# Optimization experiments

Hardware: AMD Instinct MI355X
Metric: run time of the kernel (lower is better)

Reference implementation:

```python
import jax, jax.numpy as jnp
import numpy as np

# dims
N, E, C, KV, H, OUT, MID, L = 8192, 32768, 32, 8, 8, 16, 64, 2
KVT = 2 * KV          # fused key+value channels per degree
EDGE_DIM = 5          # 4 edge scalar channels + radial norm (get_populated_edge_features)
S = KVT * C           # radial weight block per (pair, frequency)
RAD_OUT = 6 * S       # pairs (0,0),(0,1),(1,0) x1 freq + (1,1) x3 freqs

_EPS3 = np.zeros((3, 3, 3), np.float32)
for (a, b, c) in [(0, 1, 2), (1, 2, 0), (2, 0, 1)]:
    _EPS3[a, b, c] = 1.0
for (a, b, c) in [(0, 2, 1), (2, 1, 0), (1, 0, 2)]:
    _EPS3[a, b, c] = -1.0


def _ln(x, g, b):
    mu = x.mean(-1, keepdims=True)
    v = ((x - mu) ** 2).mean(-1, keepdims=True)
    return (x - mu) / jnp.sqrt(v + 1e-5) * g + b


def _radial(es, W1, b1, g, beta, W2):
    # radial profile MLP with layer norm (use_layer_norm=True)
    return jax.nn.relu(_ln(es @ W1 + b1, g, beta)) @ W2


def _segment_softmax(logit, dst, n):
    mx = jax.ops.segment_max(logit, dst, n)
    z = jnp.exp(logit - mx[dst])
    den = jax.ops.segment_sum(z, dst, n)
    return z / (den[dst] + 1e-9)


def reference(node_feats_0, node_feats_1, edge_feats_0, rel_pos, scale, src, dst,
              rad_W1, rad_b1, rad_g, rad_beta, rad_W2, Wq0, Wq1, Wp0, Wp1,
              ng0, nb0, ng1, nb1, fin_W1, fin_b1, fin_g, fin_beta, fin_W2):
    eps3 = jnp.asarray(_EPS3)
    e, n = rel_pos.shape[0], node_feats_0.shape[0]
    # --- get_basis: spherical-harmonic / Clebsch-Gordan basis up to max_degree=1 ---
    rn = jnp.linalg.norm(rel_pos, axis=-1, keepdims=True)           # [E,1]
    rhat = rel_pos / (rn + 1e-12)                                    # [E,3]
    I3 = jnp.eye(3, dtype=rel_pos.dtype)
    Q0 = jnp.broadcast_to(I3 / jnp.sqrt(3.0), (e, 3, 3))             # J=0 for 1->1
    Q1 = jnp.einsum('abc,ec->eab', eps3, rhat) / jnp.sqrt(2.0)       # J=1 for 1->1
    Q2 = jnp.sqrt(1.5) * (rhat[:, :, None] * rhat[:, None, :] - I3 / 3.0)  # J=2
    Q11 = jnp.stack([Q0, Q1, Q2], axis=1)                            # [E,3,3,3]
    es = jnp.concatenate([rn, edge_feats_0[:, :, 0]], axis=-1)       # [E,5]
    f0, f1 = node_feats_0, node_feats_1
    for i in range(L):
        # --- ConvSE3 producing fused key||value per degree ---
        R = _radial(es, rad_W1[i], rad_b1[i], rad_g[i], rad_beta[i], rad_W2[i])
        R00 = R[:, :S].reshape(e, KVT, C)
        R01 = R[:, S:2 * S].reshape(e, KVT, C)
        R10 = R[:, 2 * S:3 * S].reshape(e, KVT, C)
        R11 = R[:, 3 * S:].reshape(e, 3, KVT, C)
        f0s, f1s = f0[src], f1[src]
        m0 = (jnp.einsum('eoc,ec->eo', R00, f0s[:, :, 0])
              + jnp.einsum('eoc,eb,ecb->eo', R10, rhat, f1s))          # [E,KVT]
        m1 = (jnp.einsum('eoc,ea,ec->eoa', R01, rhat, f0s[:, :, 0])
              + jnp.einsum('ejoc,ejab,ecb->eoa', R11, Q11, f1s))       # [E,KVT,3]
        m0 = m0 * scale[:, None]
        m1 = m1 * scale[:, None, None]
        # --- attention: keys from edges, queries from dst nodes ---
        k = jnp.concatenate([m0[:, :KV], m1[:, :KV].reshape(e, KV * 3)], -1).reshape(e, H, -1)
        q0 = jnp.einsum('ncm,ck->nkm', f0, Wq0[i])                     # [N,KV,1]
        q1 = jnp.einsum('ncm,ck->nkm', f1, Wq1[i])                     # [N,KV,3]
        q = jnp.concatenate([q0[:, :, 0], q1.reshape(n, KV * 3)], -1).reshape(n, H, -1)
        logit = (k * q[dst]).sum(-1) / np.sqrt(k.shape[-1])            # [E,H]
        a = _segment_softmax(logit, dst, n)
        v0 = m0[:, KV:].reshape(e, H, KV // H)
        v1 = m1[:, KV:].reshape(e, H, KV // H, 3)
        o0 = jax.ops.segment_sum(a[:, :, None] * v0, dst, n).reshape(n, KV, 1)
        o1 = jax.ops.segment_sum(a[:, :, None, None] * v1, dst, n).reshape(n, KV, 3)
        # --- project (attn out concat skip) ---
        f0 = jnp.einsum('ncm,co->nom', jnp.concatenate([o0, f0], 1), Wp0[i])
        f1 = jnp.einsum('ncm,co->nom', jnp.concatenate([o1, f1], 1), Wp1[i])
        # --- NormSE3: equivariant norm-gated nonlinearity ---
        n0 = jnp.sqrt((f0 ** 2).sum(-1) + 1e-12)
        f0 = f0 * (jax.nn.relu(_ln(n0, ng0[i], nb0[i])) / n0)[:, :, None]
        n1 = jnp.sqrt((f1 ** 2).sum(-1) + 1e-12)
        f1 = f1 * (jax.nn.relu(_ln(n1, ng1[i], nb1[i])) / n1)[:, :, None]
    # --- final ConvSE3 (pool=False, self_interaction=False) -> degree 0 ---
    Rf = _radial(es, fin_W1, fin_b1, fin_g, fin_beta, fin_W2)
    Rf00 = Rf[:, :OUT * C].reshape(e, OUT, C)
    Rf10 = Rf[:, OUT * C:].reshape(e, OUT, C)
    mf = (jnp.einsum('eoc,ec->eo', Rf00, f0[src][:, :, 0])
          + jnp.einsum('eoc,eb,ecb->eo', Rf10, rhat, f1[src])) * scale[:, None]
    return jax.ops.segment_sum(mf, dst, n)[:, :, None]                 # feats['0']: [N,OUT,1]


def setup_inputs():
    ks = jax.random.split(jax.random.key(0), 16)
    s = 0.1
    d = {}
    d['node_feats_0'] = jax.random.normal(ks[0], (N, C, 1), jnp.float32)
    d['node_feats_1'] = jax.random.normal(ks[1], (N, C, 3), jnp.float32)
    d['edge_feats_0'] = jax.random.normal(ks[2], (E, 4, 1), jnp.float32)
    d['rel_pos'] = jax.random.normal(ks[3], (E, 3), jnp.float32)
    d['scale'] = jax.random.uniform(ks[4], (E,), jnp.float32)
    d['src'] = jax.random.randint(ks[5], (E,), 0, N)
    d['dst'] = jax.random.randint(ks[6], (E,), 0, N)
    d['rad_W1'] = jax.random.normal(ks[7], (L, EDGE_DIM, MID), jnp.float32) * s
    d['rad_b1'] = jnp.zeros((L, MID), jnp.float32)
    d['rad_g'] = jnp.ones((L, MID), jnp.float32)
    d['rad_beta'] = jnp.zeros((L, MID), jnp.float32)
    d['rad_W2'] = jax.random.normal(ks[8], (L, MID, RAD_OUT), jnp.float32) * (s / 8)
    d['Wq0'] = jax.random.normal(ks[9], (L, C, KV), jnp.float32) * s
    d['Wq1'] = jax.random.normal(ks[10], (L, C, KV), jnp.float32) * s
    d['Wp0'] = jax.random.normal(ks[11], (L, KV + C, C), jnp.float32) * s
    d['Wp1'] = jax.random.normal(ks[12], (L, KV + C, C), jnp.float32) * s
    d['ng0'] = jnp.ones((L, C), jnp.float32)
    d['nb0'] = jnp.zeros((L, C), jnp.float32)
    d['ng1'] = jnp.ones((L, C), jnp.float32)
    d['nb1'] = jnp.zeros((L, C), jnp.float32)
    d['fin_W1'] = jax.random.normal(ks[13], (EDGE_DIM, MID), jnp.float32) * s
    d['fin_b1'] = jnp.zeros((MID,), jnp.float32)
    d['fin_g'] = jnp.ones((MID,), jnp.float32)
    d['fin_beta'] = jnp.zeros((MID,), jnp.float32)
    d['fin_W2'] = jax.random.normal(ks[14], (MID, 2 * OUT * C), jnp.float32) * (s / 8)
    return d
```

## Files before the change

kernel.cpp:

```cpp
#include <hip/hip_runtime.h>
#include <math.h>

#define NN 8192
#define NE 32768
#define CC 32
#define EB 64

typedef __attribute__((ext_vector_type(8))) short s16x8;
typedef __attribute__((ext_vector_type(4))) float f32x4;

__device__ __forceinline__ unsigned short f2bf(float f) {
  unsigned u = __float_as_uint(f);
  u += 0x7FFFu + ((u >> 16) & 1u);
  return (unsigned short)(u >> 16);
}

__device__ __forceinline__ void mfma_pair(const s16x8* __restrict__ w2v, int g, int lane,
                                          s16x8 bh0, s16x8 bh1, f32x4& D0, f32x4& D1) {
  const s16x8* ap = w2v + ((size_t)g*4*64 + lane);
  s16x8 a00 = ap[0], a01 = ap[64], a10 = ap[128], a11 = ap[192];
  f32x4 z = {0.f,0.f,0.f,0.f};
  D0 = __builtin_amdgcn_mfma_f32_16x16x32_bf16(a00, bh0, z, 0,0,0);
  D0 = __builtin_amdgcn_mfma_f32_16x16x32_bf16(a01, bh1, D0, 0,0,0);
  D1 = __builtin_amdgcn_mfma_f32_16x16x32_bf16(a10, bh0, z, 0,0,0);
  D1 = __builtin_amdgcn_mfma_f32_16x16x32_bf16(a11, bh1, D1, 0,0,0);
}

__global__ void k_prep(const float* __restrict__ rel, const float* __restrict__ ef,
                       float* __restrict__ es, float* __restrict__ rhat) {
  int e = blockIdx.x * blockDim.x + threadIdx.x;
  if (e >= NE) return;
  float x = rel[e*3+0], y = rel[e*3+1], z = rel[e*3+2];
  float rn = sqrtf(x*x + y*y + z*z);
  float inv = 1.0f / (rn + 1e-12f);
  rhat[e*3+0] = x*inv; rhat[e*3+1] = y*inv; rhat[e*3+2] = z*inv;
  es[e*5+0] = rn;
  es[e*5+1] = ef[e*4+0];
  es[e*5+2] = ef[e*4+1];
  es[e*5+3] = ef[e*4+2];
  es[e*5+4] = ef[e*4+3];
}

__global__ void k_count(const int* __restrict__ dst, int* __restrict__ cnt) {
  int e = blockIdx.x * blockDim.x + threadIdx.x;
  if (e < NE) atomicAdd(&cnt[dst[e]], 1);
}

__global__ __launch_bounds__(1024) void k_scan(const int* __restrict__ cnt,
                                               int* __restrict__ offs, int* __restrict__ cursor) {
  __shared__ int part[1024];
  int t = threadIdx.x;
  int base = t * 8;
  int loc[8];
  int s = 0;
  #pragma unroll
  for (int j = 0; j < 8; ++j) { loc[j] = s; s += cnt[base + j]; }
  part[t] = s;
  __syncthreads();
  for (int off = 1; off < 1024; off <<= 1) {
    int v = (t >= off) ? part[t - off] : 0;
    __syncthreads();
    part[t] += v;
    __syncthreads();
  }
  int pre = (t == 0) ? 0 : part[t - 1];
  #pragma unroll
  for (int j = 0; j < 8; ++j) {
    int o = pre + loc[j];
    offs[base + j] = o;
    cursor[base + j] = o;
  }
  if (t == 1023) offs[NN] = part[1023];
}

__global__ void k_fill(const int* __restrict__ dst, int* __restrict__ cursor,
                       int* __restrict__ eidx) {
  int e = blockIdx.x * blockDim.x + threadIdx.x;
  if (e >= NE) return;
  int pos = atomicAdd(&cursor[dst[e]], 1);
  eidx[pos] = e;
}

__global__ void k_radial(const float* __restrict__ es, const float* __restrict__ W1,
                         const float* __restrict__ b1, const float* __restrict__ g,
                         const float* __restrict__ be, unsigned short* __restrict__ h) {
  int t = blockIdx.x * blockDim.x + threadIdx.x;
  int e = t >> 6, m = t & 63;
  if (e >= NE) return;
  const float* ep = es + (size_t)e*5;
  float v = b1[m];
  v = fmaf(ep[0], W1[0*64+m], v);
  v = fmaf(ep[1], W1[1*64+m], v);
  v = fmaf(ep[2], W1[2*64+m], v);
  v = fmaf(ep[3], W1[3*64+m], v);
  v = fmaf(ep[4], W1[4*64+m], v);
  float s = v;
  #pragma unroll
  for (int off = 32; off; off >>= 1) s += __shfl_xor(s, off);
  float mu = s * (1.0f/64.0f);
  float d = v - mu;
  float s2 = d*d;
  #pragma unroll
  for (int off = 32; off; off >>= 1) s2 += __shfl_xor(s2, off);
  float hv = d * rsqrtf(s2*(1.0f/64.0f) + 1e-5f) * g[m] + be[m];
  h[(size_t)e*64+m] = f2bf(fmaxf(hv, 0.0f));
}

__global__ void k_w2cvt(const float* __restrict__ W2, unsigned short* __restrict__ dstp, int N) {
  int idx = blockIdx.x * blockDim.x + threadIdx.x;
  int total = (N >> 5) * 4 * 64;
  if (idx >= total) return;
  int l = idx & 63;
  int fr = idx >> 6;
  int kh = fr & 1;
  int mt = (fr >> 1) & 1;
  int g  = fr >> 2;
  int kb  = kh*32 + (l >> 4)*8;
  int col = g*32 + mt*16 + (l & 15);
  s16x8 v;
  #pragma unroll
  for (int j = 0; j < 8; ++j) v[j] = (short)f2bf(W2[(size_t)(kb + j)*N + col]);
  *reinterpret_cast<s16x8*>(dstp + (size_t)idx*8) = v;
}

__global__ __launch_bounds__(512) void k_conv_mfma(
    const unsigned short* __restrict__ hbf, const unsigned short* __restrict__ w2s,
    const float* __restrict__ f0, const float* __restrict__ f1,
    const float* __restrict__ rhat, const float* __restrict__ scale,
    const int* __restrict__ src, float* __restrict__ m_out)
{
  __shared__ float rhs[EB][4];
  __shared__ float scs[EB];
  __shared__ float macc[EB][81];
  int tid = threadIdx.x;
  int e0 = blockIdx.x * EB;

  for (int idx = tid; idx < EB; idx += 512) {
    rhs[idx][0] = rhat[(e0+idx)*3+0];
    rhs[idx][1] = rhat[(e0+idx)*3+1];
    rhs[idx][2] = rhat[(e0+idx)*3+2];
    scs[idx]    = scale[e0+idx];
  }

  int lane = tid & 63, wv = tid >> 6;
  int cl = lane & 15;
  int rb = ((lane >> 4) & 3) * 4;
  int ko = (lane >> 4) * 8;
  int et = wv & 3, gp = wv >> 2;
  int e  = et*16 + cl;

  const unsigned short* hb = hbf + (size_t)e0*64;
  s16x8 bh0 = *reinterpret_cast<const s16x8*>(hb + (size_t)e*64 + ko);
  s16x8 bh1 = *reinterpret_cast<const s16x8*>(hb + (size_t)e*64 + 32 + ko);
  const s16x8* w2v = reinterpret_cast<const s16x8*>(w2s);

  int sn = src[e0+e];
  float rx = rhat[(e0+e)*3+0], ry = rhat[(e0+e)*3+1], rz = rhat[(e0+e)*3+2];
  float F0[8], T1[8], F1r[24];
  #pragma unroll
  for (int r = 0; r < 4; ++r) {
    int cA = rb + r, cB = 16 + rb + r;
    F0[r]   = f0[(size_t)sn*32 + cA];
    F0[4+r] = f0[(size_t)sn*32 + cB];
    #pragma unroll
    for (int a = 0; a < 3; ++a) {
      F1r[r*3+a]    = f1[(size_t)sn*96 + cA*3 + a];
      F1r[12+r*3+a] = f1[(size_t)sn*96 + cB*3 + a];
    }
  }
  #pragma unroll
  for (int r = 0; r < 4; ++r) {
    T1[r]   = rx*F1r[r*3+0]    + ry*F1r[r*3+1]    + rz*F1r[r*3+2];
    T1[4+r] = rx*F1r[12+r*3+0] + ry*F1r[12+r*3+1] + rz*F1r[12+r*3+2];
  }

  const float inv_s3 = 0.57735026919f;
  const float inv_s2 = 0.70710678118f;
  const float c15    = 1.22474487139f;

  #pragma unroll 1
  for (int i = 0; i < 8; ++i) {
    int g = 2*i + gp;
    float m0v, qv, m1x, m1y, m1z;
    {
      f32x4 D0, D1;
      mfma_pair(w2v, g, lane, bh0, bh1, D0, D1);
      float p = 0.f;
      #pragma unroll
      for (int r = 0; r < 4; ++r) { p = fmaf(D0[r], F0[r], p); p = fmaf(D1[r], F0[4+r], p); }
      m0v = p;
    }
    {
      f32x4 D0, D1;
      mfma_pair(w2v, 16 + g, lane, bh0, bh1, D0, D1);
      float p = 0.f;
      #pragma unroll
      for (int r = 0; r < 4; ++r) { p = fmaf(D0[r], F0[r], p); p = fmaf(D1[r], F0[4+r], p); }
      qv = p;
    }
    {
      f32x4 D0, D1;
      mfma_pair(w2v, 32 + g, lane, bh0, bh1, D0, D1);
      float p = 0.f;
      #pragma unroll
      for (int r = 0; r < 4; ++r) { p = fmaf(D0[r], T1[r], p); p = fmaf(D1[r], T1[4+r], p); }
      m0v += p;
    }
    {
      f32x4 D0, D1;
      mfma_pair(w2v, 48 + g, lane, bh0, bh1, D0, D1);
      float v0=0.f, v1=0.f, v2=0.f;
      #pragma unroll
      for (int r = 0; r < 4; ++r) {
        v0 = fmaf(D0[r], F1r[r*3+0], v0); v0 = fmaf(D1[r], F1r[12+r*3+0], v0);
        v1 = fmaf(D0[r], F1r[r*3+1], v1); v1 = fmaf(D1[r], F1r[12+r*3+1], v1);
        v2 = fmaf(D0[r], F1r[r*3+2], v2); v2 = fmaf(D1[r], F1r[12+r*3+2], v2);
      }
      m1x = v0*inv_s3; m1y = v1*inv_s3; m1z = v2*inv_s3;
    }
    {
      f32x4 D0, D1;
      mfma_pair(w2v, 64 + g, lane, bh0, bh1, D0, D1);
      float v0=0.f, v1=0.f, v2=0.f;
      #pragma unroll
      for (int r = 0; r < 4; ++r) {
        v0 = fmaf(D0[r], F1r[r*3+0], v0); v0 = fmaf(D1[r], F1r[12+r*3+0], v0);
        v1 = fmaf(D0[r], F1r[r*3+1], v1); v1 = fmaf(D1[r], F1r[12+r*3+1], v1);
        v2 = fmaf(D0[r], F1r[r*3+2], v2); v2 = fmaf(D1[r], F1r[12+r*3+2], v2);
      }
      m1x += (rz*v1 - ry*v2)*inv_s2;
      m1y += (rx*v2 - rz*v0)*inv_s2;
      m1z += (ry*v0 - rx*v1)*inv_s2;
    }
    {
      f32x4 D0, D1;
      mfma_pair(w2v, 80 + g, lane, bh0, bh1, D0, D1);
      float v0=0.f, v1=0.f, v2=0.f, w=0.f;
      #pragma unroll
      for (int r = 0; r < 4; ++r) {
        v0 = fmaf(D0[r], F1r[r*3+0], v0); v0 = fmaf(D1[r], F1r[12+r*3+0], v0);
        v1 = fmaf(D0[r], F1r[r*3+1], v1); v1 = fmaf(D1[r], F1r[12+r*3+1], v1);
        v2 = fmaf(D0[r], F1r[r*3+2], v2); v2 = fmaf(D1[r], F1r[12+r*3+2], v2);
        w  = fmaf(D0[r], T1[r], w);       w  = fmaf(D1[r], T1[4+r], w);
      }
      m1x += c15*(rx*w - v0*(1.0f/3.0f));
      m1y += c15*(ry*w - v1*(1.0f/3.0f));
      m1z += c15*(rz*w - v2*(1.0f/3.0f));
    }
    m0v += __shfl_xor(m0v, 16); m0v += __shfl_xor(m0v, 32);
    qv  += __shfl_xor(qv,  16); qv  += __shfl_xor(qv,  32);
    m1x += __shfl_xor(m1x, 16); m1x += __shfl_xor(m1x, 32);
    m1y += __shfl_xor(m1y, 16); m1y += __shfl_xor(m1y, 32);
    m1z += __shfl_xor(m1z, 16); m1z += __shfl_xor(m1z, 32);
    if (lane < 16) {
      macc[e][g]          = m0v;
      macc[e][16 + g]     = qv;
      macc[e][32 + g*3+0] = m1x;
      macc[e][32 + g*3+1] = m1y;
      macc[e][32 + g*3+2] = m1z;
    }
  }
  __syncthreads();
  for (int idx = tid; idx < EB*64; idx += 512) {
    int e2 = idx >> 6, t2 = idx & 63;
    float sc = scs[e2];
    float val;
    if (t2 < 16) {
      val = macc[e2][t2] * sc;
    } else {
      int o = (t2-16)/3, a2 = (t2-16)%3;
      val = (macc[e2][32 + (t2-16)] + macc[e2][16+o]*rhs[e2][a2]) * sc;
    }
    m_out[(size_t)(e0+e2)*64 + t2] = val;
  }
}

__global__ void k_query(const float* __restrict__ f0, const float* __restrict__ f1,
                        const float* __restrict__ Wq0, const float* __restrict__ Wq1,
                        float* __restrict__ q) {
  int n = blockIdx.x * blockDim.x + threadIdx.x;
  if (n >= NN) return;
  float q0[8]  = {0,0,0,0,0,0,0,0};
  float q1x[8] = {0,0,0,0,0,0,0,0};
  float q1y[8] = {0,0,0,0,0,0,0,0};
  float q1z[8] = {0,0,0,0,0,0,0,0};
  for (int c = 0; c < 32; ++c) {
    float fv = f0[(size_t)n*32+c];
    float fx = f1[(size_t)n*96+c*3+0];
    float fy = f1[(size_t)n*96+c*3+1];
    float fz = f1[(size_t)n*96+c*3+2];
    #pragma unroll
    for (int k = 0; k < 8; ++k) {
      float w0 = Wq0[c*8+k], w1 = Wq1[c*8+k];
      q0[k]  = fmaf(fv, w0, q0[k]);
      q1x[k] = fmaf(fx, w1, q1x[k]);
      q1y[k] = fmaf(fy, w1, q1y[k]);
      q1z[k] = fmaf(fz, w1, q1z[k]);
    }
  }
  #pragma unroll
  for (int k = 0; k < 8; ++k) {
    q[(size_t)n*32+k]         = q0[k];
    q[(size_t)n*32+8+k*3+0]   = q1x[k];
    q[(size_t)n*32+8+k*3+1]   = q1y[k];
    q[(size_t)n*32+8+k*3+2]   = q1z[k];
  }
}

__global__ void k_attn(const float* __restrict__ m, const float* __restrict__ q,
                       const int* __restrict__ offs, const int* __restrict__ eidx,
                       float* __restrict__ o0, float* __restrict__ o1) {
  int idx = blockIdx.x * blockDim.x + threadIdx.x;
  int n = idx >> 3, h = idx & 7;
  if (n >= NN) return;
  const float* qd = q + (size_t)n*32 + 4*h;
  float q0 = qd[0], q1 = qd[1], q2 = qd[2], q3 = qd[3];
  int kb = (h < 2) ? 4*h : 8 + 4*h;
  int b0 = offs[n], b1 = offs[n+1];
  float M = -3.4e38f, D = 0.f, A0 = 0.f, Ax = 0.f, Ay = 0.f, Az = 0.f;
  for (int j = b0; j < b1; ++j) {
    int e = eidx[j];
    const float* me = m + (size_t)e*64;
    float4 kv = *reinterpret_cast<const float4*>(me + kb);
    float l = 0.5f * (kv.x*q0 + kv.y*q1 + kv.z*q2 + kv.w*q3);
    float v0 = me[8+h];
    float vx = me[40+3*h], vy = me[41+3*h], vz = me[42+3*h];
    if (l > M) {
      float sc = __expf(M - l);
      D *= sc; A0 *= sc; Ax *= sc; Ay *= sc; Az *= sc;
      M = l;
    }
    float z = __expf(l - M);
    D += z;
    A0 = fmaf(z, v0, A0);
    Ax = fmaf(z, vx, Ax);
    Ay = fmaf(z, vy, Ay);
    Az = fmaf(z, vz, Az);
  }
  float inv = 1.0f / (D + 1e-9f);
  o0[(size_t)n*8+h] = A0*inv;
  o1[(size_t)n*24+3*h+0] = Ax*inv;
  o1[(size_t)n*24+3*h+1] = Ay*inv;
  o1[(size_t)n*24+3*h+2] = Az*inv;
}

__global__ void k_update(const float* __restrict__ o0, const float* __restrict__ o1,
                         const float* __restrict__ f0c, const float* __restrict__ f1c,
                         const float* __restrict__ Wp0, const float* __restrict__ Wp1,
                         const float* __restrict__ ng0v, const float* __restrict__ nb0v,
                         const float* __restrict__ ng1v, const float* __restrict__ nb1v,
                         float* __restrict__ f0o, float* __restrict__ f1o) {
  int t = blockIdx.x * blockDim.x + threadIdx.x;
  int n = t >> 5, o = t & 31;
  if (n >= NN) return;
  float a0 = 0.0f, ax = 0.0f, ay = 0.0f, az = 0.0f;
  for (int c = 0; c < 8; ++c) {
    float w0 = Wp0[c*32+o], w1 = Wp1[c*32+o];
    a0 = fmaf(o0[(size_t)n*8+c], w0, a0);
    ax = fmaf(o1[(size_t)n*24+c*3+0], w1, ax);
    ay = fmaf(o1[(size_t)n*24+c*3+1], w1, ay);
    az = fmaf(o1[(size_t)n*24+c*3+2], w1, az);
  }
  for (int c = 0; c < 32; ++c) {
    float w0 = Wp0[(8+c)*32+o], w1 = Wp1[(8+c)*32+o];
    a0 = fmaf(f0c[(size_t)n*32+c], w0, a0);
    ax = fmaf(f1c[(size_t)n*96+c*3+0], w1, ax);
    ay = fmaf(f1c[(size_t)n*96+c*3+1], w1, ay);
    az = fmaf(f1c[(size_t)n*96+c*3+2], w1, az);
  }
  float nn0 = sqrtf(a0*a0 + 1e-12f);
  float nn1 = sqrtf(ax*ax + ay*ay + az*az + 1e-12f);
  float s0 = nn0, s1 = nn1;
  #pragma unroll
  for (int off = 16; off; off >>= 1) { s0 += __shfl_xor(s0, off, 32); s1 += __shfl_xor(s1, off, 32); }
  float mu0 = s0*(1.0f/32.0f), mu1 = s1*(1.0f/32.0f);
  float d0 = nn0 - mu0, d1 = nn1 - mu1;
  float v0 = d0*d0, v1 = d1*d1;
  #pragma unroll
  for (int off = 16; off; off >>= 1) { v0 += __shfl_xor(v0, off, 32); v1 += __shfl_xor(v1, off, 32); }
  float g0 = fmaxf(d0*rsqrtf(v0*(1.0f/32.0f)+1e-5f)*ng0v[o] + nb0v[o], 0.0f) / nn0;
  float g1 = fmaxf(d1*rsqrtf(v1*(1.0f/32.0f)+1e-5f)*ng1v[o] + nb1v[o], 0.0f) / nn1;
  f0o[(size_t)n*32+o] = a0*g0;
  f1o[(size_t)n*96+o*3+0] = ax*g1;
  f1o[(size_t)n*96+o*3+1] = ay*g1;
  f1o[(size_t)n*96+o*3+2] = az*g1;
}

__global__ __launch_bounds__(512) void k_fconv_mfma(
    const unsigned short* __restrict__ hbf, const unsigned short* __restrict__ w2s,
    const float* __restrict__ f0, const float* __restrict__ f1,
    const float* __restrict__ rhat, const float* __restrict__ scale,
    const int* __restrict__ src, const int* __restrict__ dst, float* __restrict__ out)
{
  __shared__ float macc[EB][17];
  __shared__ float scs[EB];
  int tid = threadIdx.x;
  int e0 = blockIdx.x * EB;

  for (int idx = tid; idx < EB; idx += 512) scs[idx] = scale[e0+idx];

  int lane = tid & 63, wv = tid >> 6;
  int cl = lane & 15;
  int rb = ((lane >> 4) & 3) * 4;
  int ko = (lane >> 4) * 8;
  int et = wv & 3, gp = wv >> 2;
  int e  = et*16 + cl;

  const unsigned short* hb = hbf + (size_t)e0*64;
  s16x8 bh0 = *reinterpret_cast<const s16x8*>(hb + (size_t)e*64 + ko);
  s16x8 bh1 = *reinterpret_cast<const s16x8*>(hb + (size_t)e*64 + 32 + ko);
  const s16x8* w2v = reinterpret_cast<const s16x8*>(w2s);

  int sn = src[e0+e];
  float rx = rhat[(e0+e)*3+0], ry = rhat[(e0+e)*3+1], rz = rhat[(e0+e)*3+2];
  float F0[8], T1[8];
  #pragma unroll
  for (int r = 0; r < 4; ++r) {
    int cA = rb + r, cB = 16 + rb + r;
    F0[r]   = f0[(size_t)sn*32 + cA];
    F0[4+r] = f0[(size_t)sn*32 + cB];
    float ax0 = f1[(size_t)sn*96 + cA*3 + 0];
    float ax1 = f1[(size_t)sn*96 + cA*3 + 1];
    float ax2 = f1[(size_t)sn*96 + cA*3 + 2];
    float bx0 = f1[(size_t)sn*96 + cB*3 + 0];
    float bx1 = f1[(size_t)sn*96 + cB*3 + 1];
    float bx2 = f1[(size_t)sn*96 + cB*3 + 2];
    T1[r]   = rx*ax0 + ry*ax1 + rz*ax2;
    T1[4+r] = rx*bx0 + ry*bx1 + rz*bx2;
  }

  #pragma unroll 1
  for (int i = 0; i < 8; ++i) {
    int g = 2*i + gp;
    float am;
    {
      f32x4 D0, D1;
      mfma_pair(w2v, g, lane, bh0, bh1, D0, D1);
      float p = 0.f;
      #pragma unroll
      for (int r = 0; r < 4; ++r) { p = fmaf(D0[r], F0[r], p); p = fmaf(D1[r], F0[4+r], p); }
      am = p;
    }
    {
      f32x4 D0, D1;
      mfma_pair(w2v, 16 + g, lane, bh0, bh1, D0, D1);
      float p = 0.f;
      #pragma unroll
      for (int r = 0; r < 4; ++r) { p = fmaf(D0[r], T1[r], p); p = fmaf(D1[r], T1[4+r], p); }
      am += p;
    }
    am += __shfl_xor(am, 16); am += __shfl_xor(am, 32);
    if (lane < 16) macc[e][g] = am;
  }
  __syncthreads();
  for (int idx = tid; idx < EB*16; idx += 512) {
    int e2 = idx >> 4, o = idx & 15;
    atomicAdd(&out[(size_t)dst[e0+e2]*16 + o], macc[e2][o]*scs[e2]);
  }
}

extern "C" void kernel_launch(void* const* d_in, const int* in_sizes, int n_in,
                              void* d_out, int out_size, void* d_ws, size_t ws_size,
                              hipStream_t stream) {
  (void)in_sizes; (void)n_in; (void)ws_size;
  const float* nf0  = (const float*)d_in[0];
  const float* nf1  = (const float*)d_in[1];
  const float* ef0  = (const float*)d_in[2];
  const float* rel  = (const float*)d_in[3];
  const float* scale= (const float*)d_in[4];
  const int*   src  = (const int*)d_in[5];
  const int*   dst  = (const int*)d_in[6];
  const float* rW1  = (const float*)d_in[7];
  const float* rb1  = (const float*)d_in[8];
  const float* rg   = (const float*)d_in[9];
  const float* rbe  = (const float*)d_in[10];
  const float* rW2  = (const float*)d_in[11];
  const float* Wq0  = (const float*)d_in[12];
  const float* Wq1  = (const float*)d_in[13];
  const float* Wp0  = (const float*)d_in[14];
  const float* Wp1  = (const float*)d_in[15];
  const float* ng0  = (const float*)d_in[16];
  const float* nb0  = (const float*)d_in[17];
  const float* ng1  = (const float*)d_in[18];
  const float* nb1  = (const float*)d_in[19];
  const float* fW1  = (const float*)d_in[20];
  const float* fb1  = (const float*)d_in[21];
  const float* fg   = (const float*)d_in[22];
  const float* fbe  = (const float*)d_in[23];
  const float* fW2  = (const float*)d_in[24];

  float* ws = (float*)d_ws;
  size_t off = 0;
  float* es    = ws + off; off += (size_t)NE*5;
  float* rhat  = ws + off; off += (size_t)NE*3;
  float* m     = ws + off; off += (size_t)NE*64;
  float* q     = ws + off; off += (size_t)NN*32;
  float* o0    = ws + off; off += (size_t)NN*8;
  float* o1    = ws + off; off += (size_t)NN*24;
  float* f0a   = ws + off; off += (size_t)NN*32;
  float* f1a   = ws + off; off += (size_t)NN*96;
  float* f0b   = ws + off; off += (size_t)NN*32;
  float* f1b   = ws + off; off += (size_t)NN*96;
  int* cnt     = (int*)(ws + off); off += NN;
  int* offs    = (int*)(ws + off); off += NN + 1;
  int* cursor  = (int*)(ws + off); off += NN;
  int* eidx    = (int*)(ws + off); off += NE;
  unsigned short* usbase = (unsigned short*)(ws + off);
  unsigned short* hbf  = usbase;
  unsigned short* w2s0 = hbf  + (size_t)NE*64;
  unsigned short* w2s1 = w2s0 + 196608;
  unsigned short* w2sf = w2s1 + 196608;

  hipMemsetAsync(cnt, 0, NN*sizeof(int), stream);
  k_count<<<NE/256, 256, 0, stream>>>(dst, cnt);
  k_scan<<<1, 1024, 0, stream>>>(cnt, offs, cursor);
  k_fill<<<NE/256, 256, 0, stream>>>(dst, cursor, eidx);

  k_w2cvt<<<96, 256, 0, stream>>>(rW2,            w2s0, 3072);
  k_w2cvt<<<96, 256, 0, stream>>>(rW2 + 64*3072,  w2s1, 3072);
  k_w2cvt<<<32, 256, 0, stream>>>(fW2,            w2sf, 1024);

  k_prep<<<NE/256, 256, 0, stream>>>(rel, ef0, es, rhat);

  const float* f0c = nf0; const float* f1c = nf1;
  float* f0n = f0a; float* f1n = f1a;
  for (int l = 0; l < 2; ++l) {
    k_radial<<<NE*64/256, 256, 0, stream>>>(es, rW1 + l*320, rb1 + l*64, rg + l*64, rbe + l*64, hbf);
    k_conv_mfma<<<NE/EB, 512, 0, stream>>>(hbf, (l == 0) ? w2s0 : w2s1, f0c, f1c, rhat, scale, src, m);
    k_query<<<NN/256, 256, 0, stream>>>(f0c, f1c, Wq0 + l*256, Wq1 + l*256, q);
    k_attn<<<NN*8/256, 256, 0, stream>>>(m, q, offs, eidx, o0, o1);
    k_update<<<NN*32/256, 256, 0, stream>>>(o0, o1, f0c, f1c, Wp0 + l*1280, Wp1 + l*1280,
                                            ng0 + l*32, nb0 + l*32, ng1 + l*32, nb1 + l*32,
                                            f0n, f1n);
    f0c = f0n; f1c = f1n; f0n = f0b; f1n = f1b;
  }
  k_radial<<<NE*64/256, 256, 0, stream>>>(es, fW1, fb1, fg, fbe, hbf);
  hipMemsetAsync(d_out, 0, (size_t)out_size*sizeof(float), stream);
  k_fconv_mfma<<<NE/EB, 512, 0, stream>>>(hbf, w2sf, f0c, f1c, rhat, scale, src, dst, (float*)d_out);
}
```

Baseline: 292.2 us.

## Fuse radial MLP into conv kernels and merge query/attention/update per layer

Computes the radial MLP hidden layer inside each conv kernel and keeps it in shared memory instead of writing a bf16 buffer to global memory. The query, attention and update kernels are merged into one block-per-32-nodes kernel that passes intermediates through shared memory. The three weight conversion launches become one. The aim is fewer launches and less global round-trip traffic, at the cost of more shared memory and extra redundant compute per conv block, which may reduce occupancy.

Result: faster. 257.1 us (-12.0%).

```diff
diff --git a/kernel.cpp b/kernel.cpp
--- a/kernel.cpp
+++ b/kernel.cpp
@@ -81,33 +81,15 @@
   eidx[pos] = e;
 }
 
-__global__ void k_radial(const float* __restrict__ es, const float* __restrict__ W1,
-                         const float* __restrict__ b1, const float* __restrict__ g,
-                         const float* __restrict__ be, unsigned short* __restrict__ h) {
-  int t = blockIdx.x * blockDim.x + threadIdx.x;
-  int e = t >> 6, m = t & 63;
-  if (e >= NE) return;
-  const float* ep = es + (size_t)e*5;
-  float v = b1[m];
-  v = fmaf(ep[0], W1[0*64+m], v);
-  v = fmaf(ep[1], W1[1*64+m], v);
-  v = fmaf(ep[2], W1[2*64+m], v);
-  v = fmaf(ep[3], W1[3*64+m], v);
-  v = fmaf(ep[4], W1[4*64+m], v);
-  float s = v;
-  #pragma unroll
-  for (int off = 32; off; off >>= 1) s += __shfl_xor(s, off);
-  float mu = s * (1.0f/64.0f);
-  float d = v - mu;
-  float s2 = d*d;
-  #pragma unroll
-  for (int off = 32; off; off >>= 1) s2 += __shfl_xor(s2, off);
-  float hv = d * rsqrtf(s2*(1.0f/64.0f) + 1e-5f) * g[m] + be[m];
-  h[(size_t)e*64+m] = f2bf(fmaxf(hv, 0.0f));
-}
-
-__global__ void k_w2cvt(const float* __restrict__ W2, unsigned short* __restrict__ dstp, int N) {
-  int idx = blockIdx.x * blockDim.x + threadIdx.x;
+__global__ void k_w2all(const float* __restrict__ W2a, const float* __restrict__ W2b,
+                        const float* __restrict__ W2f,
+                        unsigned short* __restrict__ d0, unsigned short* __restrict__ d1,
+                        unsigned short* __restrict__ df) {
+  int b = blockIdx.x;
+  const float* src; unsigned short* dstp; int N; int idx;
+  if (b < 96)       { src = W2a; dstp = d0; N = 3072; idx = b*256 + threadIdx.x; }
+  else if (b < 192) { src = W2b; dstp = d1; N = 3072; idx = (b-96)*256 + threadIdx.x; }
+  else              { src = W2f; dstp = df; N = 1024; idx = (b-192)*256 + threadIdx.x; }
   int total = (N >> 5) * 4 * 64;
   if (idx >= total) return;
   int l = idx & 63;
@@ -119,12 +101,14 @@
   int col = g*32 + mt*16 + (l & 15);
   s16x8 v;
   #pragma unroll
-  for (int j = 0; j < 8; ++j) v[j] = (short)f2bf(W2[(size_t)(kb + j)*N + col]);
+  for (int j = 0; j < 8; ++j) v[j] = (short)f2bf(src[(size_t)(kb + j)*N + col]);
   *reinterpret_cast<s16x8*>(dstp + (size_t)idx*8) = v;
 }
 
 __global__ __launch_bounds__(512) void k_conv_mfma(
-    const unsigned short* __restrict__ hbf, const unsigned short* __restrict__ w2s,
+    const float* __restrict__ es, const float* __restrict__ W1,
+    const float* __restrict__ b1, const float* __restrict__ gm,
+    const float* __restrict__ be, const unsigned short* __restrict__ w2s,
     const float* __restrict__ f0, const float* __restrict__ f1,
     const float* __restrict__ rhat, const float* __restrict__ scale,
     const int* __restrict__ src, float* __restrict__ m_out)
@@ -132,8 +116,10 @@
   __shared__ float rhs[EB][4];
   __shared__ float scs[EB];
   __shared__ float macc[EB][81];
+  __shared__ unsigned short hs[EB][72];
   int tid = threadIdx.x;
   int e0 = blockIdx.x * EB;
+  int lane = tid & 63, wv = tid >> 6;
 
   for (int idx = tid; idx < EB; idx += 512) {
     rhs[idx][0] = rhat[(e0+idx)*3+0];
@@ -142,20 +128,46 @@
     scs[idx]    = scale[e0+idx];
   }
 
-  int lane = tid & 63, wv = tid >> 6;
+  {
+    float w1v0 = W1[0*64+lane], w1v1 = W1[1*64+lane], w1v2 = W1[2*64+lane];
+    float w1v3 = W1[3*64+lane], w1v4 = W1[4*64+lane];
+    float b1v = b1[lane], gv = gm[lane], bev = be[lane];
+    #pragma unroll
+    for (int j = 0; j < 8; ++j) {
+      int ee = wv*8 + j;
+      const float* ep = es + (size_t)(e0+ee)*5;
+      float v = b1v;
+      v = fmaf(ep[0], w1v0, v);
+      v = fmaf(ep[1], w1v1, v);
+      v = fmaf(ep[2], w1v2, v);
+      v = fmaf(ep[3], w1v3, v);
+      v = fmaf(ep[4], w1v4, v);
+      float s = v;
+      #pragma unroll
+      for (int off = 32; off; off >>= 1) s += __shfl_xor(s, off);
+      float mu = s * (1.0f/64.0f);
+      float d = v - mu;
+      float s2 = d*d;
+      #pragma unroll
+      for (int off = 32; off; off >>= 1) s2 += __shfl_xor(s2, off);
+      float hv = d * rsqrtf(s2*(1.0f/64.0f) + 1e-5f) * gv + bev;
+      hs[ee][lane] = f2bf(fmaxf(hv, 0.0f));
+    }
+  }
+  __syncthreads();
+
   int cl = lane & 15;
   int rb = ((lane >> 4) & 3) * 4;
   int ko = (lane >> 4) * 8;
   int et = wv & 3, gp = wv >> 2;
   int e  = et*16 + cl;
 
-  const unsigned short* hb = hbf + (size_t)e0*64;
-  s16x8 bh0 = *reinterpret_cast<const s16x8*>(hb + (size_t)e*64 + ko);
-  s16x8 bh1 = *reinterpret_cast<const s16x8*>(hb + (size_t)e*64 + 32 + ko);
+  s16x8 bh0 = *reinterpret_cast<const s16x8*>(&hs[e][ko]);
+  s16x8 bh1 = *reinterpret_cast<const s16x8*>(&hs[e][32 + ko]);
   const s16x8* w2v = reinterpret_cast<const s16x8*>(w2s);
 
   int sn = src[e0+e];
-  float rx = rhat[(e0+e)*3+0], ry = rhat[(e0+e)*3+1], rz = rhat[(e0+e)*3+2];
+  float rx = rhs[e][0], ry = rhs[e][1], rz = rhs[e][2];
   float F0[8], T1[8], F1r[24];
   #pragma unroll
   for (int r = 0; r < 4; ++r) {
@@ -275,140 +287,165 @@
   }
 }
 
-__global__ void k_query(const float* __restrict__ f0, const float* __restrict__ f1,
-                        const float* __restrict__ Wq0, const float* __restrict__ Wq1,
-                        float* __restrict__ q) {
-  int n = blockIdx.x * blockDim.x + threadIdx.x;
-  if (n >= NN) return;
-  float q0[8]  = {0,0,0,0,0,0,0,0};
-  float q1x[8] = {0,0,0,0,0,0,0,0};
-  float q1y[8] = {0,0,0,0,0,0,0,0};
-  float q1z[8] = {0,0,0,0,0,0,0,0};
-  for (int c = 0; c < 32; ++c) {
-    float fv = f0[(size_t)n*32+c];
-    float fx = f1[(size_t)n*96+c*3+0];
-    float fy = f1[(size_t)n*96+c*3+1];
-    float fz = f1[(size_t)n*96+c*3+2];
+__global__ __launch_bounds__(256) void k_qau(
+    const float* __restrict__ f0c, const float* __restrict__ f1c,
+    const float* __restrict__ Wq0, const float* __restrict__ Wq1,
+    const float* __restrict__ m, const int* __restrict__ offs, const int* __restrict__ eidx,
+    const float* __restrict__ Wp0, const float* __restrict__ Wp1,
+    const float* __restrict__ ng0v, const float* __restrict__ nb0v,
+    const float* __restrict__ ng1v, const float* __restrict__ nb1v,
+    float* __restrict__ f0o, float* __restrict__ f1o)
+{
+  __shared__ float qs[32][33];
+  __shared__ float os0[32][9];
+  __shared__ float os1[32][25];
+  int tid = threadIdx.x;
+  int n0 = blockIdx.x * 32;
+
+  {
+    int nl = tid >> 3, k = tid & 7;
+    int n = n0 + nl;
+    float a0 = 0.f, ax = 0.f, ay = 0.f, az = 0.f;
+    for (int c = 0; c < 32; ++c) {
+      float w0 = Wq0[c*8+k], w1 = Wq1[c*8+k];
+      a0 = fmaf(f0c[(size_t)n*32+c], w0, a0);
+      ax = fmaf(f1c[(size_t)n*96+c*3+0], w1, ax);
+      ay = fmaf(f1c[(size_t)n*96+c*3+1], w1, ay);
+      az = fmaf(f1c[(size_t)n*96+c*3+2], w1, az);
+    }
+    qs[nl][k]       = a0;
+    qs[nl][8+k*3+0] = ax;
+    qs[nl][8+k*3+1] = ay;
+    qs[nl][8+k*3+2] = az;
+  }
+  __syncthreads();
+
+  {
+    int nl = tid >> 3, h = tid & 7;
+    int n = n0 + nl;
+    float q0 = qs[nl][4*h+0], q1 = qs[nl][4*h+1], q2 = qs[nl][4*h+2], q3 = qs[nl][4*h+3];
+    int kb = (h < 2) ? 4*h : 8 + 4*h;
+    int b0 = offs[n], b1 = offs[n+1];
+    float M = -3.4e38f, D = 0.f, A0 = 0.f, Ax = 0.f, Ay = 0.f, Az = 0.f;
+    for (int j = b0; j < b1; ++j) {
+      int e = eidx[j];
+      const float* me = m + (size_t)e*64;
+      float4 kv = *reinterpret_cast<const float4*>(me + kb);
+      float l = 0.5f * (kv.x*q0 + kv.y*q1 + kv.z*q2 + kv.w*q3);
+      float v0 = me[8+h];
+      float vx = me[40+3*h], vy = me[41+3*h], vz = me[42+3*h];
+      if (l > M) {
+        float sc = __expf(M - l);
+        D *= sc; A0 *= sc; Ax *= sc; Ay *= sc; Az *= sc;
+        M = l;
+      }
+      float z = __expf(l - M);
+      D += z;
+      A0 = fmaf(z, v0, A0);
+      Ax = fmaf(z, vx, Ax);
+      Ay = fmaf(z, vy, Ay);
+      Az = fmaf(z, vz, Az);
+    }
+    float inv = 1.0f / (D + 1e-9f);
+    os0[nl][h]     = A0*inv;
+    os1[nl][3*h+0] = Ax*inv;
+    os1[nl][3*h+1] = Ay*inv;
+    os1[nl][3*h+2] = Az*inv;
+  }
+  __syncthreads();
+
+  #pragma unroll 1
+  for (int p = 0; p < 4; ++p) {
+    int nl = p*8 + (tid >> 5), o = tid & 31;
+    int n = n0 + nl;
+    float a0 = 0.f, ax = 0.f, ay = 0.f, az = 0.f;
     #pragma unroll
-    for (int k = 0; k < 8; ++k) {
-      float w0 = Wq0[c*8+k], w1 = Wq1[c*8+k];
-      q0[k]  = fmaf(fv, w0, q0[k]);
-      q1x[k] = fmaf(fx, w1, q1x[k]);
-      q1y[k] = fmaf(fy, w1, q1y[k]);
-      q1z[k] = fmaf(fz, w1, q1z[k]);
-    }
-  }
-  #pragma unroll
-  for (int k = 0; k < 8; ++k) {
-    q[(size_t)n*32+k]         = q0[k];
-    q[(size_t)n*32+8+k*3+0]   = q1x[k];
-    q[(size_t)n*32+8+k*3+1]   = q1y[k];
-    q[(size_t)n*32+8+k*3+2]   = q1z[k];
-  }
-}
-
-__global__ void k_attn(const float* __restrict__ m, const float* __restrict__ q,
-                       const int* __restrict__ offs, const int* __restrict__ eidx,
-                       float* __restrict__ o0, float* __restrict__ o1) {
-  int idx = blockIdx.x * blockDim.x + threadIdx.x;
-  int n = idx >> 3, h = idx & 7;
-  if (n >= NN) return;
-  const float* qd = q + (size_t)n*32 + 4*h;
-  float q0 = qd[0], q1 = qd[1], q2 = qd[2], q3 = qd[3];
-  int kb = (h < 2) ? 4*h : 8 + 4*h;
-  int b0 = offs[n], b1 = offs[n+1];
-  float M = -3.4e38f, D = 0.f, A0 = 0.f, Ax = 0.f, Ay = 0.f, Az = 0.f;
-  for (int j = b0; j < b1; ++j) {
-    int e = eidx[j];
-    const float* me = m + (size_t)e*64;
-    float4 kv = *reinterpret_cast<const float4*>(me + kb);
-    float l = 0.5f * (kv.x*q0 + kv.y*q1 + kv.z*q2 + kv.w*q3);
-    float v0 = me[8+h];
-    float vx = me[40+3*h], vy = me[41+3*h], vz = me[42+3*h];
-    if (l > M) {
-      float sc = __expf(M - l);
-      D *= sc; A0 *= sc; Ax *= sc; Ay *= sc; Az *= sc;
-      M = l;
-    }
-    float z = __expf(l - M);
-    D += z;
-    A0 = fmaf(z, v0, A0);
-    Ax = fmaf(z, vx, Ax);
-    Ay = fmaf(z, vy, Ay);
-    Az = fmaf(z, vz, Az);
-  }
-  float inv = 1.0f / (D + 1e-9f);
-  o0[(size_t)n*8+h] = A0*inv;
-  o1[(size_t)n*24+3*h+0] = Ax*inv;
-  o1[(size_t)n*24+3*h+1] = Ay*inv;
-  o1[(size_t)n*24+3*h+2] = Az*inv;
-}
-
-__global__ void k_update(const float* __restrict__ o0, const float* __restrict__ o1,
-                         const float* __restrict__ f0c, const float* __restrict__ f1c,
-                         const float* __restrict__ Wp0, const float* __restrict__ Wp1,
-                         const float* __restrict__ ng0v, const float* __restrict__ nb0v,
-                         const float* __restrict__ ng1v, const float* __restrict__ nb1v,
-                         float* __restrict__ f0o, float* __restrict__ f1o) {
-  int t = blockIdx.x * blockDim.x + threadIdx.x;
-  int n = t >> 5, o = t & 31;
-  if (n >= NN) return;
-  float a0 = 0.0f, ax = 0.0f, ay = 0.0f, az = 0.0f;
-  for (int c = 0; c < 8; ++c) {
-    float w0 = Wp0[c*32+o], w1 = Wp1[c*32+o];
-    a0 = fmaf(o0[(size_t)n*8+c], w0, a0);
-    ax = fmaf(o1[(size_t)n*24+c*3+0], w1, ax);
-    ay = fmaf(o1[(size_t)n*24+c*3+1], w1, ay);
-    az = fmaf(o1[(size_t)n*24+c*3+2], w1, az);
-  }
-  for (int c = 0; c < 32; ++c) {
-    float w0 = Wp0[(8+c)*32+o], w1 = Wp1[(8+c)*32+o];
-    a0 = fmaf(f0c[(size_t)n*32+c], w0, a0);
-    ax = fmaf(f1c[(size_t)n*96+c*3+0], w1, ax);
-    ay = fmaf(f1c[(size_t)n*96+c*3+1], w1, ay);
-    az = fmaf(f1c[(size_t)n*96+c*3+2], w1, az);
-  }
-  float nn0 = sqrtf(a0*a0 + 1e-12f);
-  float nn1 = sqrtf(ax*ax + ay*ay + az*az + 1e-12f);
-  float s0 = nn0, s1 = nn1;
-  #pragma unroll
-  for (int off = 16; off; off >>= 1) { s0 += __shfl_xor(s0, off, 32); s1 += __shfl_xor(s1, off, 32); }
-  float mu0 = s0*(1.0f/32.0f), mu1 = s1*(1.0f/32.0f);
-  float d0 = nn0 - mu0, d1 = nn1 - mu1;
-  float v0 = d0*d0, v1 = d1*d1;
-  #pragma unroll
-  for (int off = 16; off; off >>= 1) { v0 += __shfl_xor(v0, off, 32); v1 += __shfl_xor(v1, off, 32); }
-  float g0 = fmaxf(d0*rsqrtf(v0*(1.0f/32.0f)+1e-5f)*ng0v[o] + nb0v[o], 0.0f) / nn0;
-  float g1 = fmaxf(d1*rsqrtf(v1*(1.0f/32.0f)+1e-5f)*ng1v[o] + nb1v[o], 0.0f) / nn1;
-  f0o[(size_t)n*32+o] = a0*g0;
-  f1o[(size_t)n*96+o*3+0] = ax*g1;
-  f1o[(size_t)n*96+o*3+1] = ay*g1;
-  f1o[(size_t)n*96+o*3+2] = az*g1;
+    for (int c = 0; c < 8; ++c) {
+      float w0 = Wp0[c*32+o], w1 = Wp1[c*32+o];
+      a0 = fmaf(os0[nl][c], w0, a0);
+      ax = fmaf(os1[nl][c*3+0], w1, ax);
+      ay = fmaf(os1[nl][c*3+1], w1, ay);
+      az = fmaf(os1[nl][c*3+2], w1, az);
+    }
+    for (int c = 0; c < 32; ++c) {
+      float w0 = Wp0[(8+c)*32+o], w1 = Wp1[(8+c)*32+o];
+      a0 = fmaf(f0c[(size_t)n*32+c], w0, a0);
+      ax = fmaf(f1c[(size_t)n*96+c*3+0], w1, ax);
+      ay = fmaf(f1c[(size_t)n*96+c*3+1], w1, ay);
+      az = fmaf(f1c[(size_t)n*96+c*3+2], w1, az);
+    }
+    float nn0 = sqrtf(a0*a0 + 1e-12f);
+    float nn1 = sqrtf(ax*ax + ay*ay + az*az + 1e-12f);
+    float s0 = nn0, s1 = nn1;
+    #pragma unroll
+    for (int off = 16; off; off >>= 1) { s0 += __shfl_xor(s0, off, 32); s1 += __shfl_xor(s1, off, 32); }
+    float mu0 = s0*(1.0f/32.0f), mu1 = s1*(1.0f/32.0f);
+    float d0 = nn0 - mu0, d1 = nn1 - mu1;
+    float v0 = d0*d0, v1 = d1*d1;
+    #pragma unroll
+    for (int off = 16; off; off >>= 1) { v0 += __shfl_xor(v0, off, 32); v1 += __shfl_xor(v1, off, 32); }
+    float g0 = fmaxf(d0*rsqrtf(v0*(1.0f/32.0f)+1e-5f)*ng0v[o] + nb0v[o], 0.0f) / nn0;
+    float g1 = fmaxf(d1*rsqrtf(v1*(1.0f/32.0f)+1e-5f)*ng1v[o] + nb1v[o], 0.0f) / nn1;
+    f0o[(size_t)n*32+o] = a0*g0;
+    f1o[(size_t)n*96+o*3+0] = ax*g1;
+    f1o[(size_t)n*96+o*3+1] = ay*g1;
+    f1o[(size_t)n*96+o*3+2] = az*g1;
+  }
 }
 
 __global__ __launch_bounds__(512) void k_fconv_mfma(
-    const unsigned short* __restrict__ hbf, const unsigned short* __restrict__ w2s,
+    const float* __restrict__ es, const float* __restrict__ W1,
+    const float* __restrict__ b1, const float* __restrict__ gm,
+    const float* __restrict__ be, const unsigned short* __restrict__ w2s,
     const float* __restrict__ f0, const float* __restrict__ f1,
     const float* __restrict__ rhat, const float* __restrict__ scale,
     const int* __restrict__ src, const int* __restrict__ dst, float* __restrict__ out)
 {
   __shared__ float macc[EB][17];
   __shared__ float scs[EB];
+  __shared__ unsigned short hs[EB][72];
   int tid = threadIdx.x;
   int e0 = blockIdx.x * EB;
+  int lane = tid & 63, wv = tid >> 6;
 
   for (int idx = tid; idx < EB; idx += 512) scs[idx] = scale[e0+idx];
 
-  int lane = tid & 63, wv = tid >> 6;
+  {
+    float w1v0 = W1[0*64+lane], w1v1 = W1[1*64+lane], w1v2 = W1[2*64+lane];
+    float w1v3 = W1[3*64+lane], w1v4 = W1[4*64+lane];
+    float b1v = b1[lane], gv = gm[lane], bev = be[lane];
+    #pragma unroll
+    for (int j = 0; j < 8; ++j) {
+      int ee = wv*8 + j;
+      const float* ep = es + (size_t)(e0+ee)*5;
+      float v = b1v;
+      v = fmaf(ep[0], w1v0, v);
+      v = fmaf(ep[1], w1v1, v);
+      v = fmaf(ep[2], w1v2, v);
+      v = fmaf(ep[3], w1v3, v);
+      v = fmaf(ep[4], w1v4, v);
+      float s = v;
+      #pragma unroll
+      for (int off = 32; off; off >>= 1) s += __shfl_xor(s, off);
+      float mu = s * (1.0f/64.0f);
+      float d = v - mu;
+      float s2 = d*d;
+      #pragma unroll
+      for (int off = 32; off; off >>= 1) s2 += __shfl_xor(s2, off);
+      float hv = d * rsqrtf(s2*(1.0f/64.0f) + 1e-5f) * gv + bev;
+      hs[ee][lane] = f2bf(fmaxf(hv, 0.0f));
+    }
+  }
+  __syncthreads();
+
   int cl = lane & 15;
   int rb = ((lane >> 4) & 3) * 4;
   int ko = (lane >> 4) * 8;
   int et = wv & 3, gp = wv >> 2;
   int e  = et*16 + cl;
 
-  const unsigned short* hb = hbf + (size_t)e0*64;
-  s16x8 bh0 = *reinterpret_cast<const s16x8*>(hb + (size_t)e*64 + ko);
-  s16x8 bh1 = *reinterpret_cast<const s16x8*>(hb + (size_t)e*64 + 32 + ko);
+  s16x8 bh0 = *reinterpret_cast<const s16x8*>(&hs[e][ko]);
+  s16x8 bh1 = *reinterpret_cast<const s16x8*>(&hs[e][32 + ko]);
   const s16x8* w2v = reinterpret_cast<const s16x8*>(w2s);
 
   int sn = src[e0+e];
@@ -494,9 +531,6 @@
   float* es    = ws + off; off += (size_t)NE*5;
   float* rhat  = ws + off; off += (size_t)NE*3;
   float* m     = ws + off; off += (size_t)NE*64;
-  float* q     = ws + off; off += (size_t)NN*32;
-  float* o0    = ws + off; off += (size_t)NN*8;
-  float* o1    = ws + off; off += (size_t)NN*24;
   float* f0a   = ws + off; off += (size_t)NN*32;
   float* f1a   = ws + off; off += (size_t)NN*96;
   float* f0b   = ws + off; off += (size_t)NN*32;
@@ -506,8 +540,7 @@
   int* cursor  = (int*)(ws + off); off += NN;
   int* eidx    = (int*)(ws + off); off += NE;
   unsigned short* usbase = (unsigned short*)(ws + off);
-  unsigned short* hbf  = usbase;
-  unsigned short* w2s0 = hbf  + (size_t)NE*64;
+  unsigned short* w2s0 = usbase;
   unsigned short* w2s1 = w2s0 + 196608;
   unsigned short* w2sf = w2s1 + 196608;
 
@@ -516,25 +549,22 @@
   k_scan<<<1, 1024, 0, stream>>>(cnt, offs, cursor);
   k_fill<<<NE/256, 256, 0, stream>>>(dst, cursor, eidx);
 
-  k_w2cvt<<<96, 256, 0, stream>>>(rW2,            w2s0, 3072);
-  k_w2cvt<<<96, 256, 0, stream>>>(rW2 + 64*3072,  w2s1, 3072);
-  k_w2cvt<<<32, 256, 0, stream>>>(fW2,            w2sf, 1024);
+  k_w2all<<<224, 256, 0, stream>>>(rW2, rW2 + 64*3072, fW2, w2s0, w2s1, w2sf);
 
   k_prep<<<NE/256, 256, 0, stream>>>(rel, ef0, es, rhat);
 
   const float* f0c = nf0; const float* f1c = nf1;
   float* f0n = f0a; float* f1n = f1a;
   for (int l = 0; l < 2; ++l) {
-    k_radial<<<NE*64/256, 256, 0, stream>>>(es, rW1 + l*320, rb1 + l*64, rg + l*64, rbe + l*64, hbf);
-    k_conv_mfma<<<NE/EB, 512, 0, stream>>>(hbf, (l == 0) ? w2s0 : w2s1, f0c, f1c, rhat, scale, src, m);
-    k_query<<<NN/256, 256, 0, stream>>>(f0c, f1c, Wq0 + l*256, Wq1 + l*256, q);
-    k_attn<<<NN*8/256, 256, 0, stream>>>(m, q, offs, eidx, o0, o1);
-    k_update<<<NN*32/256, 256, 0, stream>>>(o0, o1, f0c, f1c, Wp0 + l*1280, Wp1 + l*1280,
-                                            ng0 + l*32, nb0 + l*32, ng1 + l*32, nb1 + l*32,
-                                            f0n, f1n);
+    k_conv_mfma<<<NE/EB, 512, 0, stream>>>(es, rW1 + l*320, rb1 + l*64, rg + l*64, rbe + l*64,
+                                           (l == 0) ? w2s0 : w2s1, f0c, f1c, rhat, scale, src, m);
+    k_qau<<<NN/32, 256, 0, stream>>>(f0c, f1c, Wq0 + l*256, Wq1 + l*256, m, offs, eidx,
+                                     Wp0 + l*1280, Wp1 + l*1280,
+                                     ng0 + l*32, nb0 + l*32, ng1 + l*32, nb1 + l*32,
+                                     f0n, f1n);
     f0c = f0n; f1c = f1n; f0n = f0b; f1n = f1b;
   }
-  k_radial<<<NE*64/256, 256, 0, stream>>>(es, fW1, fb1, fg, fbe, hbf);
   hipMemsetAsync(d_out, 0, (size_t)out_size*sizeof(float), stream);
-  k_fconv_mfma<<<NE/EB, 512, 0, stream>>>(hbf, w2sf, f0c, f1c, rhat, scale, src, dst, (float*)d_out);
-}
+  k_fconv_mfma<<<NE/EB, 512, 0, stream>>>(es, fW1, fb1, fg, fbe, w2sf,
+                                          f0c, f1c, rhat, scale, src, dst, (float*)d_out);
+}
```
